# Kernel tuning notes

Measured on AMD Instinct MI355X. Metric: run time of the kernel, lower is better.

The kernel has to match this reference:

```python
import jax, jax.numpy as jnp
from jax import lax
import numpy as np

K = 3  # kernel size per dim, dimension=6 -> 3**6 = 729 taps
OFFS = np.stack(np.meshgrid(*([np.arange(K)] * 6), indexing='ij'), axis=-1).reshape(-1, 6).astype(np.int32)


def conv6d(x, kernel):
    """Dense emulation of a 1->1 channel MinkowskiConvolution over 6 spatial dims.

    x: (b, s, s, d, d, d, d) with zeros at absent sparse coordinates.
    kernel: (729,) flattened 3^6 kernel (in=out=1 channel, no bias).
    Zeros at absent coordinates contribute nothing to the gathered sums, so the
    dense conv equals the sparse conv evaluated everywhere.
    """
    xp = jnp.pad(x, [(0, 0)] + [(1, 1)] * 6)
    offs = jnp.asarray(OFFS)
    zero = jnp.int32(0)

    def body(acc, ow):
        off, wt = ow
        sl = lax.dynamic_slice(
            xp, (zero, off[0], off[1], off[2], off[3], off[4], off[5]), x.shape)
        return acc + wt * sl, None

    acc, _ = lax.scan(jax.checkpoint(body), jnp.zeros_like(x), (offs, kernel))
    return acc


def _transpose6d(t):
    # swap the two scale dims and the two image-coordinate pairs:
    # (b, s1, s2, h1, w1, h2, w2) -> (b, s2, s1, h2, w2, h1, w1)
    return jnp.transpose(t, (0, 2, 1, 5, 6, 3, 4))


def setup_inputs() -> dict:
    key = jax.random.key(0)
    k1, k2 = jax.random.split(key)
    x = jax.random.normal(k1, (1, 2, 2, 32, 32, 32, 32), dtype=jnp.float32)
    kernel = jax.random.normal(k2, (K ** 6,), dtype=jnp.float32) * 0.05
    return {"x": x, "kernel": kernel}


def reference(x, kernel):
    # MinkowskiConvolution outputs at the input coordinate set; MinkowskiSigmoid
    # acts on features at those coordinates; to_dense() zero-fills elsewhere.
    # Dense equivalent: mask to the input nonzero set.
    mask = (x != 0).astype(x.dtype)
    branch = lambda z: jax.nn.sigmoid(conv6d(jax.nn.relu(z), kernel))
    # symmetric mode: conv(x) + T(conv(T(x))); T(coords(T(x))) == coords(x)
    y = mask * (branch(x) + _transpose6d(branch(_transpose6d(x))))
    b, s1, s2, d1, d2, d3, d4 = y.shape
    y = y.reshape(b, s1 * s2, d1, d2, d3, d4).sum(axis=1)  # (b, h1, w1, h2, w2)
    return y
```

## Files before the change

### kernel.cpp

```cpp
#include <hip/hip_runtime.h>

typedef _Float16 half8 __attribute__((ext_vector_type(8)));
typedef float f16v __attribute__((ext_vector_type(16)));
typedef float f4 __attribute__((ext_vector_type(4)));
typedef unsigned long long ull;

#define X_SLAB   1048576
#define PLANE_BYTES (34*36*4*2)
#define RPT_SITES (34*34*34*36)
#define RPT_OFF  65536
#define RPT_SLACK 4096
#define MSK_OFF  (RPT_OFF + RPT_SITES*8 + RPT_SLACK)
#define TAB_N    (3*6*3*512)
#define TAB_ELEMS  (4*81*8)

__global__ __launch_bounds__(256)
void prep(const float* __restrict__ x, const float* __restrict__ w,
          ull* __restrict__ rpt, unsigned char* __restrict__ mskb,
          _Float16* __restrict__ tabm) {
    unsigned s = blockIdx.x * 256 + threadIdx.x;
    if (s < RPT_SITES) {
        unsigned q = s;
        int j4 = q % 36; q /= 36;
        int j3 = q % 34; q /= 34;
        int j2 = q % 34; q /= 34;
        int j1 = q;
        union { _Float16 h[4]; ull u; } pk;
        pk.u = 0ull;
        if (j1 >= 1 && j1 <= 32 && j2 >= 1 && j2 <= 32 &&
            j3 >= 1 && j3 <= 32 && j4 >= 1 && j4 <= 32) {
            size_t off = (size_t)(j1-1)*32768 + (j2-1)*1024 + (j3-1)*32 + (j4-1);
            unsigned nib = 0;
            #pragma unroll
            for (int t = 0; t < 4; ++t) {
                float v = x[(size_t)t*X_SLAB + off];
                nib |= (v != 0.f ? 1u : 0u) << t;
                pk.h[t] = (_Float16)fmaxf(v, 0.f);
            }
            mskb[off] = (unsigned char)nib;
        }
        rpt[s] = pk.u;
    }
    if (blockIdx.x == 0) {
        for (int idx = threadIdx.x; idx < TAB_N; idx += 256) {
            int j = idx & 7, l = (idx >> 3) & 63, slice = idx >> 9;
            int p4 = slice % 3, j2rel = (slice/3) % 6, p2 = slice/18;
            int n32 = l & 31;
            int d2 = n32 >> 3, n8 = n32 & 7;
            int k = 8*(l>>5) + j;
            int p5h = k >> 2, t = k & 3;
            int p3 = j2rel - d2;
            float val = 0.f;
            if (p5h < 3 && p3 >= 0 && p3 <= 2) {
                int br = n8 & 1, sc = n8 >> 1, s1 = sc >> 1, s2 = sc & 1;
                int t1 = t >> 1, t2 = t & 1;
                int a = t1 - s1 + 1, b = t2 - s2 + 1;
                int widx = (br == 0)
                    ? (a*243 + b*81 + p2*27 + p3*9 + p4*3 + p5h)
                    : (b*243 + a*81 + p4*27 + p5h*9 + p2*3 + p3);
                val = w[widx];
            }
            tabm[idx] = (_Float16)val;
        }
    }
}

__global__ __launch_bounds__(256)
void conv_mfma(const ull* __restrict__ rpt, const unsigned char* __restrict__ mskb,
               const _Float16* __restrict__ tabm, float* __restrict__ out) {
    __shared__ __align__(16) unsigned char stg[4][2][2048];

    const int tid  = threadIdx.x;
    const int lane = tid & 63;
    const int wv   = tid >> 6;
    const int e2b  = blockIdx.x * 4;
    const int e1   = blockIdx.y;
    const int bz   = blockIdx.z;

    f16v acc[2];
    #pragma unroll
    for (int r = 0; r < 2; ++r)
        #pragma unroll
        for (int i = 0; i < 16; ++i) acc[r][i] = 0.f;

    const int R     = bz*8 + wv*2;
    const int j4off = (lane & 31)*8 + (lane >> 5)*16;
    const char* aglob0 = (const char*)rpt + (size_t)R*288 + lane*16;

    auto stage_to = [&](int it, int slot) {
        int p2 = it / 6, j2 = it - p2*6;
        const char* src = aglob0 + ((size_t)(e1+p2)*34 + (e2b+j2))*PLANE_BYTES;
        unsigned char* dst = &stg[wv][slot][0] + lane*16;
        #pragma unroll
        for (int k = 0; k < 2; ++k)
            __builtin_amdgcn_global_load_lds(
                (const __attribute__((address_space(1))) unsigned int*)(src + k*1024),
                (__attribute__((address_space(3))) unsigned int*)(dst + k*1024),
                16, 0, 0);
    };
    auto loadB = [&](int it, half8* B) {
        const _Float16* tb = tabm + it*1536 + lane*8;
        B[0] = *(const half8*)(tb);
        B[1] = *(const half8*)(tb + 512);
        B[2] = *(const half8*)(tb + 1024);
    };
    auto compute = [&](int slot, const half8* B) {
        const unsigned char* sb = &stg[wv][slot][0];
        union { ull u[2]; half8 h; } A[4];
        #pragma unroll
        for (int j3l = 0; j3l < 4; ++j3l) {
            const ull* ap = (const ull*)(sb + j3l*288 + j4off);
            A[j3l].u[0] = ap[0];
            A[j3l].u[1] = ap[1];
        }
        #pragma unroll
        for (int p4 = 0; p4 < 3; ++p4) {
            acc[0] = __builtin_amdgcn_mfma_f32_32x32x16_f16(A[p4  ].h, B[p4], acc[0], 0,0,0);
            acc[1] = __builtin_amdgcn_mfma_f32_32x32x16_f16(A[p4+1].h, B[p4], acc[1], 0,0,0);
        }
    };

    half8 Ba[3], Bb[3];
    stage_to(0, 0);
    loadB(0, Ba);

    #pragma unroll 1
    for (int ip = 0; ip < 9; ++ip) {
        const int itE = 2*ip;
        {
            stage_to(itE + 1, 1);
            loadB(itE + 1, Bb);
            asm volatile("s_waitcnt vmcnt(5)" ::: "memory");
            compute(0, Ba);
        }
        {
            int nit = (itE + 2 < 18) ? itE + 2 : 17;
            stage_to(nit, 0);
            loadB(nit, Ba);
            asm volatile("s_waitcnt vmcnt(5)" ::: "memory");
            compute(1, Bb);
        }
    }

    const int n8 = lane & 7;
    const int d2 = (lane >> 3) & 3;
    const int h  = lane >> 5;
    const int sbit = n8 >> 1;
    const size_t colbase = (size_t)e1*32768 + (size_t)(e2b + d2)*1024;
    #pragma unroll
    for (int rloc = 0; rloc < 2; ++rloc) {
        const int e3 = R + rloc;
        float v[16];
        #pragma unroll
        for (int g = 0; g < 4; ++g) {
            unsigned mw = *(const unsigned*)&mskb[colbase + e3*32 + 8*g + 4*h];
            #pragma unroll
            for (int j = 0; j < 4; ++j) {
                float a  = acc[rloc][4*g + j];
                float sg = __builtin_amdgcn_rcpf(1.f + __expf(-a));
                v[4*g+j] = ((mw >> (8*j + sbit)) & 1u) ? sg : 0.f;
            }
        }
        #pragma unroll
        for (int i = 0; i < 16; ++i) {
            v[i] += __shfl_xor(v[i], 1);
            v[i] += __shfl_xor(v[i], 2);
            v[i] += __shfl_xor(v[i], 4);
        }
        if (n8 == 0) {
            #pragma unroll
            for (int g = 0; g < 4; ++g) {
                f4 o; o.x = v[4*g]; o.y = v[4*g+1]; o.z = v[4*g+2]; o.w = v[4*g+3];
                *(f4*)(out + colbase + e3*32 + 8*g + 4*h) = o;
            }
        }
    }
}

__global__ void build_wtab(const float* __restrict__ w, float* __restrict__ tab) {
    int idx = blockIdx.x * blockDim.x + threadIdx.x;
    if (idx >= TAB_ELEMS) return;
    int n  = idx & 7;
    int r  = idx >> 3;
    int p5 = r % 3; r /= 3;
    int p4 = r % 3; r /= 3;
    int p3 = r % 3; r /= 3;
    int p2 = r % 3; r /= 3;
    int t  = r;
    int t1 = t >> 1, t2 = t & 1;
    int br = n & 1;
    int s  = n >> 1;
    int s1 = s >> 1, s2 = s & 1;
    int a = t1 - s1 + 1;
    int b = t2 - s2 + 1;
    int widx = (br == 0)
        ? (a*243 + b*81 + p2*27 + p3*9 + p4*3 + p5)
        : (b*243 + a*81 + p4*27 + p5*9 + p2*3 + p3);
    tab[idx] = w[widx];
}

__global__ __launch_bounds__(256)
void conv_fp32(const float* __restrict__ x,
               const float* __restrict__ tab,
               float* __restrict__ out) {
    const int e4 = threadIdx.x;
    const int e3 = blockIdx.x * 8 + threadIdx.y;
    const int e2 = blockIdx.y;
    const int e1 = blockIdx.z;

    float acc[8];
    #pragma unroll
    for (int n = 0; n < 8; ++n) acc[n] = 0.f;

    #pragma unroll 1
    for (int t = 0; t < 4; ++t) {
        const float* st  = x + (size_t)t * X_SLAB;
        const float* wt0 = tab + t * 648;
        #pragma unroll
        for (int p2 = 0; p2 < 3; ++p2) {
            #pragma unroll
            for (int p3 = 0; p3 < 3; ++p3) {
                int i1 = e1 + p2 - 1, i2 = e2 + p3 - 1;
                bool v12 = ((unsigned)i1 < 32u) && ((unsigned)i2 < 32u);
                const float* base = st + (i1*32768 + i2*1024 + (e3-1)*32 + (e4-1));
                const float* wt = wt0 + (p2*3 + p3) * 72;
                #pragma unroll
                for (int p4 = 0; p4 < 3; ++p4) {
                    int i3 = e3 + p4 - 1;
                    bool v3 = v12 && ((unsigned)i3 < 32u);
                    #pragma unroll
                    for (int p5 = 0; p5 < 3; ++p5) {
                        int i4 = e4 + p5 - 1;
                        bool ok = v3 && ((unsigned)i4 < 32u);
                        float v = ok ? fmaxf(base[p4*32 + p5], 0.f) : 0.f;
                        const float* w8 = wt + (p4*3 + p5)*8;
                        #pragma unroll
                        for (int n = 0; n < 8; ++n)
                            acc[n] = fmaf(w8[n], v, acc[n]);
                    }
                }
            }
        }
    }

    const size_t eflat = (size_t)e1*32768 + e2*1024 + e3*32 + e4;
    float res = 0.f;
    #pragma unroll
    for (int i = 0; i < 4; ++i) {
        float xv = x[(size_t)i * X_SLAB + eflat];
        float s0 = __builtin_amdgcn_rcpf(1.f + __expf(-acc[2*i]));
        float s1 = __builtin_amdgcn_rcpf(1.f + __expf(-acc[2*i+1]));
        float m  = (xv != 0.f) ? 1.f : 0.f;
        res = fmaf(m, s0 + s1, res);
    }
    out[eflat] = res;
}

extern "C" void kernel_launch(void* const* d_in, const int* in_sizes, int n_in,
                              void* d_out, int out_size, void* d_ws, size_t ws_size,
                              hipStream_t stream) {
    const float* x = (const float*)d_in[0];
    const float* w = (const float*)d_in[1];
    float* out = (float*)d_out;

    const size_t need = (size_t)MSK_OFF + (size_t)X_SLAB;

    if (ws_size >= need) {
        _Float16*      tabm = (_Float16*)d_ws;
        ull*           rpt  = (ull*)((char*)d_ws + RPT_OFF);
        unsigned char* mskb = (unsigned char*)d_ws + MSK_OFF;
        prep<<<dim3((RPT_SITES + 255)/256), dim3(256), 0, stream>>>(x, w, rpt, mskb, tabm);
        dim3 grd(8, 32, 4), blk(256, 1, 1);
        conv_mfma<<<grd, blk, 0, stream>>>(rpt, mskb, tabm, out);
    } else {
        float* tab = (float*)d_ws;
        build_wtab<<<dim3((TAB_ELEMS + 255)/256), dim3(256), 0, stream>>>(w, tab);
        dim3 blk(32, 8, 1), grd(4, 32, 32);
        conv_fp32<<<grd, blk, 0, stream>>>(x, tab, out);
    }
}
```

Measured before the change: 98.14 us.

## Load A operands directly to registers with triple-buffered prefetch instead of LDS staging

Replaces the global_load_lds staging of A tiles through shared memory with direct per-lane global loads into registers. The main loop becomes fully unrolled with a 3-deep register ring that prefetches two iterations ahead. This removes the LDS round trip and the manual vmcnt waits, leaving scheduling to the compiler. The cost is more VGPR pressure, which may lower occupancy, and less coalesced 8-byte global loads.

```diff
diff --git a/kernel.cpp b/kernel.cpp
--- a/kernel.cpp
+++ b/kernel.cpp
@@ -68,8 +68,6 @@
 __global__ __launch_bounds__(256)
 void conv_mfma(const ull* __restrict__ rpt, const unsigned char* __restrict__ mskb,
                const _Float16* __restrict__ tabm, float* __restrict__ out) {
-    __shared__ __align__(16) unsigned char stg[4][2][2048];
-
     const int tid  = threadIdx.x;
     const int lane = tid & 63;
     const int wv   = tid >> 6;
@@ -85,61 +83,51 @@
 
     const int R     = bz*8 + wv*2;
     const int j4off = (lane & 31)*8 + (lane >> 5)*16;
-    const char* aglob0 = (const char*)rpt + (size_t)R*288 + lane*16;
-
-    auto stage_to = [&](int it, int slot) {
+    const char* aglob0 = (const char*)rpt + (size_t)R*288 + j4off;
+
+    ull   Ar[3][4][2];
+    half8 Bq[3][3];
+
+    auto loadA = [&](int it, int buf) {
         int p2 = it / 6, j2 = it - p2*6;
-        const char* src = aglob0 + ((size_t)(e1+p2)*34 + (e2b+j2))*PLANE_BYTES;
-        unsigned char* dst = &stg[wv][slot][0] + lane*16;
-        #pragma unroll
-        for (int k = 0; k < 2; ++k)
-            __builtin_amdgcn_global_load_lds(
-                (const __attribute__((address_space(1))) unsigned int*)(src + k*1024),
-                (__attribute__((address_space(3))) unsigned int*)(dst + k*1024),
-                16, 0, 0);
+        const char* aptr = aglob0 + ((size_t)(e1+p2)*34 + (e2b+j2))*PLANE_BYTES;
+        #pragma unroll
+        for (int j3l = 0; j3l < 4; ++j3l) {
+            const ull* ap = (const ull*)(aptr + j3l*288);
+            Ar[buf][j3l][0] = ap[0];
+            Ar[buf][j3l][1] = ap[1];
+        }
     };
-    auto loadB = [&](int it, half8* B) {
+    auto loadB = [&](int it, int buf) {
         const _Float16* tb = tabm + it*1536 + lane*8;
-        B[0] = *(const half8*)(tb);
-        B[1] = *(const half8*)(tb + 512);
-        B[2] = *(const half8*)(tb + 1024);
+        Bq[buf][0] = *(const half8*)(tb);
+        Bq[buf][1] = *(const half8*)(tb + 512);
+        Bq[buf][2] = *(const half8*)(tb + 1024);
     };
-    auto compute = [&](int slot, const half8* B) {
-        const unsigned char* sb = &stg[wv][slot][0];
+    auto compute = [&](int buf) {
         union { ull u[2]; half8 h; } A[4];
         #pragma unroll
         for (int j3l = 0; j3l < 4; ++j3l) {
-            const ull* ap = (const ull*)(sb + j3l*288 + j4off);
-            A[j3l].u[0] = ap[0];
-            A[j3l].u[1] = ap[1];
+            A[j3l].u[0] = Ar[buf][j3l][0];
+            A[j3l].u[1] = Ar[buf][j3l][1];
         }
         #pragma unroll
         for (int p4 = 0; p4 < 3; ++p4) {
-            acc[0] = __builtin_amdgcn_mfma_f32_32x32x16_f16(A[p4  ].h, B[p4], acc[0], 0,0,0);
-            acc[1] = __builtin_amdgcn_mfma_f32_32x32x16_f16(A[p4+1].h, B[p4], acc[1], 0,0,0);
+            acc[0] = __builtin_amdgcn_mfma_f32_32x32x16_f16(A[p4  ].h, Bq[buf][p4], acc[0], 0,0,0);
+            acc[1] = __builtin_amdgcn_mfma_f32_32x32x16_f16(A[p4+1].h, Bq[buf][p4], acc[1], 0,0,0);
         }
     };
 
-    half8 Ba[3], Bb[3];
-    stage_to(0, 0);
-    loadB(0, Ba);
-
-    #pragma unroll 1
-    for (int ip = 0; ip < 9; ++ip) {
-        const int itE = 2*ip;
-        {
-            stage_to(itE + 1, 1);
-            loadB(itE + 1, Bb);
-            asm volatile("s_waitcnt vmcnt(5)" ::: "memory");
-            compute(0, Ba);
-        }
-        {
-            int nit = (itE + 2 < 18) ? itE + 2 : 17;
-            stage_to(nit, 0);
-            loadB(nit, Ba);
-            asm volatile("s_waitcnt vmcnt(5)" ::: "memory");
-            compute(1, Bb);
-        }
+    loadA(0, 0); loadB(0, 0);
+    loadA(1, 1); loadB(1, 1);
+
+    #pragma unroll
+    for (int it = 0; it < 18; ++it) {
+        const int nit = (it + 2 < 18) ? it + 2 : 17;
+        const int nb  = (it + 2) % 3;
+        loadA(nit, nb);
+        loadB(nit, nb);
+        compute(it % 3);
     }
 
     const int n8 = lane & 7;
```

Result: no change. 99.86 us (+1.8%).
